# Kernel optimization log

Measured on AMD Instinct MI355X. Metric: run time of the kernel, lower is better.

The kernel has to match this reference:

```python
import jax, jax.numpy as jnp
import numpy as np
import math

DIM = 1024
N_HEADS = 16
HEAD_DIM = DIM // N_HEADS


def rope(x):
    # x: [B, H, S, D] with D == HEAD_DIM, interleaved even/odd rotation
    S = x.shape[-2]
    D = x.shape[-1]
    pos = jnp.arange(S, dtype=x.dtype)[:, None]              # [S, 1]
    dim = jnp.arange(D // 2, dtype=x.dtype)[None, :]         # [1, D/2]
    theta = pos / jnp.exp(2.0 * dim / D * math.log(10000.0))  # [S, D/2]
    sin = jnp.sin(theta)[None, None]                          # [1,1,S,D/2]
    cos = jnp.cos(theta)[None, None]
    x1 = x[..., ::2]
    x2 = x[..., 1::2]
    out1 = x1 * cos - x2 * sin
    out2 = x1 * sin + x2 * cos
    # interleave back: stack on last axis then flatten pairs
    return jnp.stack([out1, out2], axis=-1).reshape(x.shape)


def setup_inputs() -> dict:
    key = jax.random.key(0)
    ks = jax.random.split(key, 9)
    B, S = 2, 2048
    s = 1.0 / math.sqrt(DIM)
    inp = {
        "x": jax.random.normal(ks[0], (B, S, DIM), dtype=jnp.float32),
        "wq": jax.random.normal(ks[1], (DIM, DIM), dtype=jnp.float32) * s,
        "bq": jnp.zeros((DIM,), dtype=jnp.float32),
        "wk": jax.random.normal(ks[2], (DIM, DIM), dtype=jnp.float32) * s,
        "bk": jnp.zeros((DIM,), dtype=jnp.float32),
        "wv": jax.random.normal(ks[3], (DIM, DIM), dtype=jnp.float32) * s,
        "bv": jnp.zeros((DIM,), dtype=jnp.float32),
        "wo": jax.random.normal(ks[4], (DIM, DIM), dtype=jnp.float32) * s,
        "bo": jnp.zeros((DIM,), dtype=jnp.float32),
    }
    return inp


def reference(x, wq, bq, wk, bk, wv, bv, wo, bo):
    B, S, _ = x.shape
    # torch Linear: y = x @ W^T + b
    def proj(w, b):
        y = jnp.einsum('bsd,ed->bse', x, w) + b
        return y.reshape(B, S, N_HEADS, HEAD_DIM).transpose(0, 2, 1, 3)  # [B,H,S,Dh]
    q = rope(proj(wq, bq))
    k = rope(proj(wk, bk))
    v = proj(wv, bv)
    score = jnp.einsum('bhqd,bhkd->bhqk', q, k) / math.sqrt(HEAD_DIM)
    causal = jnp.tril(jnp.ones((S, S), dtype=bool))
    score = jnp.where(causal[None, None], score, -jnp.inf)
    attn = jax.nn.softmax(score, axis=-1)
    out = jnp.einsum('bhqk,bhkd->bhqd', attn, v)
    out = out.transpose(0, 2, 1, 3).reshape(B, S, DIM)
    return jnp.einsum('bsd,ed->bse', out, wo) + bo
```

## Files before the change

kernel.cpp:

```cpp
#include <hip/hip_runtime.h>
#include <cstdint>
#include <cstddef>


typedef __bf16 bf16_t;
typedef __bf16 bf16x8 __attribute__((ext_vector_type(8)));
typedef __bf16 bf16x4 __attribute__((ext_vector_type(4)));
typedef float  f32x4  __attribute__((ext_vector_type(4)));

#define DEVFN __device__ __forceinline__

static constexpr int Bn  = 2;
static constexpr int S   = 2048;
static constexpr int DIM = 1024;
static constexpr int NH  = 16;
static constexpr int HD  = 64;
static constexpr int Mrows = Bn * S;

DEVFN f32x4 mfma16(bf16x8 a, bf16x8 b, f32x4 c) {
  return __builtin_amdgcn_mfma_f32_16x16x32_bf16(a, b, c, 0, 0, 0);
}

DEVFN void gl_lds16(const bf16_t* g, bf16_t* l) {
  __builtin_amdgcn_global_load_lds(
      (const __attribute__((address_space(1))) unsigned*)g,
      (__attribute__((address_space(3))) unsigned*)l, 16, 0, 0);
}

__global__ __launch_bounds__(256) void k_prep(
    const float* __restrict__ x, const float* __restrict__ wq,
    const float* __restrict__ wk, const float* __restrict__ wv,
    const float* __restrict__ wo, bf16_t* __restrict__ xb,
    bf16_t* __restrict__ wqb, bf16_t* __restrict__ wkb,
    bf16_t* __restrict__ wvb, bf16_t* __restrict__ wob,
    float2* __restrict__ tab) {
  const int bid = blockIdx.x;
  if (bid < 8192) {
    const float* src;
    bf16_t* dst;
    size_t base;
    if (bid < 4096) {
      src = x; dst = xb; base = (size_t)bid << 10;
    } else {
      int wsel = (bid - 4096) >> 10;
      src = wsel == 0 ? wq : wsel == 1 ? wk : wsel == 2 ? wv : wo;
      dst = wsel == 0 ? wqb : wsel == 1 ? wkb : wsel == 2 ? wvb : wob;
      base = (size_t)((bid - 4096) & 1023) << 10;
    }
    size_t i = base + (size_t)threadIdx.x * 4;
    float4 v = *(const float4*)(src + i);
    bf16x4 o = { (bf16_t)v.x, (bf16_t)v.y, (bf16_t)v.z, (bf16_t)v.w };
    *(bf16x4*)(dst + i) = o;
  } else {
    int i = (bid - 8192) * 256 + threadIdx.x;
    int s = i >> 5, d = i & 31;
    float th = (float)s * expf((float)d * -0.2878231366f);
    tab[i] = make_float2(cosf(th), sinf(th));
  }
}

__global__ __launch_bounds__(256) void k_rope(bf16_t* __restrict__ X,
                                              const float2* __restrict__ tab,
                                              float scale) {
  int i = blockIdx.x * 256 + threadIdx.x;
  int row = i >> 7;
  int s = row & (S - 1);
  int dd = (i & 7) << 3;
  int p0 = dd >> 1;
  bf16x8 v = *(bf16x8*)(X + (size_t)i * 8);
  bf16x8 o;
#pragma unroll
  for (int j = 0; j < 4; ++j) {
    float x1 = (float)v[2 * j], x2 = (float)v[2 * j + 1];
    float2 cs = tab[s * 32 + p0 + j];
    o[2 * j]     = (bf16_t)((x1 * cs.x - x2 * cs.y) * scale);
    o[2 * j + 1] = (bf16_t)((x1 * cs.y + x2 * cs.x) * scale);
  }
  *(bf16x8*)(X + (size_t)i * 8) = o;
}

__global__ __launch_bounds__(256) void k_trans(const bf16_t* __restrict__ Vin,
                                               bf16_t* __restrict__ VT) {
  __shared__ __align__(16) bf16_t tile[64][72];
  int s0 = blockIdx.x * 64, bh = blockIdx.y;
  int b = bh >> 4, h = bh & 15;
  int t = threadIdx.x;
#pragma unroll
  for (int it = 0; it < 2; ++it) {
    int sl = (t >> 3) + it * 32, d0 = (t & 7) << 3;
    *(bf16x8*)&tile[sl][d0] =
        *(const bf16x8*)(Vin + (size_t)(b * S + s0 + sl) * DIM + h * HD + d0);
  }
  __syncthreads();
  int d = t >> 2, c0 = (t & 3) * 16;
  bf16_t buf[16];
#pragma unroll
  for (int j = 0; j < 16; ++j) buf[j] = tile[c0 + j][d];
  bf16_t* op = VT + ((size_t)bh * HD + d) * S + s0 + c0;
  *(bf16x8*)op = *(bf16x8*)&buf[0];
  *(bf16x8*)(op + 8) = *(bf16x8*)&buf[8];
}

DEVFN void stage64(const bf16_t* __restrict__ A, const bf16_t* __restrict__ Bw,
                   bf16_t* Al, bf16_t* Bl, int m0, int n0, int k0, int t,
                   int w) {
#pragma unroll
  for (int ld = 0; ld < 4; ++ld) {
    int c = t + ld * 256;
    int row = c >> 3;
    int j = ((c & 7) ^ (row & 7)) << 3;
    bf16_t* dstA = Al + (size_t)(w * 64 + ld * 256) * 8;
    bf16_t* dstB = Bl + (size_t)(w * 64 + ld * 256) * 8;
    gl_lds16(A + (size_t)(m0 + row) * DIM + k0 + j, dstA);
    gl_lds16(Bw + (size_t)(n0 + row) * DIM + k0 + j, dstB);
  }
}

__global__ __launch_bounds__(256) void k_gemm_qkv(
    const bf16_t* __restrict__ A, const bf16_t* __restrict__ Wall,
    const float* __restrict__ c0, const float* __restrict__ c1,
    const float* __restrict__ c2, bf16_t* __restrict__ Oq,
    bf16_t* __restrict__ Ok, bf16_t* __restrict__ Ov_) {
  __shared__ __align__(16) bf16_t Al[128 * 64];
  __shared__ __align__(16) bf16_t Bl[128 * 64];
  const int t = threadIdx.x, w = t >> 6, l = t & 63;
  const int lr = l & 15, lc = l >> 4;
  const int lid = blockIdx.x;
  const int xcd = lid & 7, s = lid >> 3;
  const int my = ((xcd >> 1) << 3) + (s & 7);
  const int nx = (xcd & 1) * 12 + (s >> 3);
  const int m0 = my * 128, n0g = nx * 128;
  const int z = n0g >> 10, n0l = n0g & 1023;
  const int wr = w >> 1, wc = w & 1;
  f32x4 acc[4][4] = {};

  for (int k0 = 0; k0 < DIM; k0 += 64) {
    __syncthreads();
    stage64(A, Wall, Al, Bl, m0, n0g, k0, t, w);
    asm volatile("s_waitcnt vmcnt(0)" ::: "memory");
    __syncthreads();
    bf16x8 af[2][4], bfr[2][4];
#pragma unroll
    for (int ks = 0; ks < 2; ++ks) {
#pragma unroll
      for (int mi = 0; mi < 4; ++mi) {
        int row = wr * 64 + mi * 16 + lr;
        int off = ((ks * 4 + lc) << 4) ^ ((row & 7) << 4);
        af[ks][mi] = *(const bf16x8*)((const char*)Al + row * 128 + off);
      }
#pragma unroll
      for (int ni = 0; ni < 4; ++ni) {
        int row = wc * 64 + ni * 16 + lr;
        int off = ((ks * 4 + lc) << 4) ^ ((row & 7) << 4);
        bfr[ks][ni] = *(const bf16x8*)((const char*)Bl + row * 128 + off);
      }
    }
    __builtin_amdgcn_s_setprio(1);
#pragma unroll
    for (int ks = 0; ks < 2; ++ks)
#pragma unroll
      for (int mi = 0; mi < 4; ++mi)
#pragma unroll
        for (int ni = 0; ni < 4; ++ni)
          acc[mi][ni] = mfma16(af[ks][mi], bfr[ks][ni], acc[mi][ni]);
    __builtin_amdgcn_s_setprio(0);
  }

  bf16_t* Ov = z == 0 ? Oq : (z == 1 ? Ok : Ov_);
  const float* bias = z == 0 ? c0 : (z == 1 ? c1 : c2);
#pragma unroll
  for (int ni = 0; ni < 4; ++ni) {
    const int col = n0l + wc * 64 + ni * 16 + lr;
    const float bv = bias[col];
#pragma unroll
    for (int mi = 0; mi < 4; ++mi)
#pragma unroll
      for (int r = 0; r < 4; ++r) {
        int row = m0 + wr * 64 + mi * 16 + lc * 4 + r;
        Ov[(size_t)row * DIM + col] = (bf16_t)(acc[mi][ni][r] + bv);
      }
  }
}

__global__ __launch_bounds__(256) void k_gemm_out(
    const bf16_t* __restrict__ A, const bf16_t* __restrict__ Bw,
    const float* __restrict__ bias, float* __restrict__ Ov) {
  __shared__ __align__(16) bf16_t Al[128 * 64];
  __shared__ __align__(16) bf16_t Bl[128 * 64];
  const int t = threadIdx.x, w = t >> 6, l = t & 63;
  const int lr = l & 15, lc = l >> 4;
  const int lid = blockIdx.x;
  const int xcd = lid & 7, s = lid >> 3;
  const int my = ((xcd >> 1) << 3) + (s & 7);
  const int nx = (xcd & 1) * 4 + (s >> 3);
  const int m0 = my * 128, n0 = nx * 128;
  const int wr = w >> 1, wc = w & 1;
  f32x4 acc[4][4] = {};

  for (int k0 = 0; k0 < DIM; k0 += 64) {
    __syncthreads();
    stage64(A, Bw, Al, Bl, m0, n0, k0, t, w);
    asm volatile("s_waitcnt vmcnt(0)" ::: "memory");
    __syncthreads();
    bf16x8 af[2][4], bfr[2][4];
#pragma unroll
    for (int ks = 0; ks < 2; ++ks) {
#pragma unroll
      for (int mi = 0; mi < 4; ++mi) {
        int row = wr * 64 + mi * 16 + lr;
        int off = ((ks * 4 + lc) << 4) ^ ((row & 7) << 4);
        af[ks][mi] = *(const bf16x8*)((const char*)Al + row * 128 + off);
      }
#pragma unroll
      for (int ni = 0; ni < 4; ++ni) {
        int row = wc * 64 + ni * 16 + lr;
        int off = ((ks * 4 + lc) << 4) ^ ((row & 7) << 4);
        bfr[ks][ni] = *(const bf16x8*)((const char*)Bl + row * 128 + off);
      }
    }
    __builtin_amdgcn_s_setprio(1);
#pragma unroll
    for (int ks = 0; ks < 2; ++ks)
#pragma unroll
      for (int mi = 0; mi < 4; ++mi)
#pragma unroll
        for (int ni = 0; ni < 4; ++ni)
          acc[mi][ni] = mfma16(af[ks][mi], bfr[ks][ni], acc[mi][ni]);
    __builtin_amdgcn_s_setprio(0);
  }

#pragma unroll
  for (int ni = 0; ni < 4; ++ni) {
    int col = n0 + wc * 64 + ni * 16 + lr;
    float bv = bias[col];
#pragma unroll
    for (int mi = 0; mi < 4; ++mi)
#pragma unroll
      for (int r = 0; r < 4; ++r) {
        int row = m0 + wr * 64 + mi * 16 + lc * 4 + r;
        Ov[(size_t)row * DIM + col] = acc[mi][ni][r] + bv;
      }
  }
}

DEVFN void stage_kv(const bf16_t* __restrict__ Kc,
                    const bf16_t* __restrict__ VT, bf16_t* Kb, bf16_t* Vb,
                    int b, int bh, int h, int k0, int tid, int w) {
#pragma unroll
  for (int ld = 0; ld < 2; ++ld) {
    int c = tid + ld * 256;
    int row = c >> 3;
    int j = ((c & 7) ^ (row & 7)) << 3;
    bf16_t* dstK = Kb + (size_t)(w * 64 + ld * 256) * 8;
    bf16_t* dstV = Vb + (size_t)(w * 64 + ld * 256) * 8;
    gl_lds16(Kc + (size_t)(b * S + k0 + row) * DIM + h * HD + j, dstK);
    gl_lds16(VT + ((size_t)bh * HD + row) * S + k0 + j, dstV);
  }
}

__global__ __launch_bounds__(256) void k_attn(const bf16_t* __restrict__ Q,
                                              const bf16_t* __restrict__ Kc,
                                              const bf16_t* __restrict__ VT,
                                              bf16_t* __restrict__ O) {
  __shared__ __align__(16) bf16_t Kl[2][64 * 64];
  __shared__ __align__(16) bf16_t Vl[3][64 * 64];
  __shared__ __align__(16) bf16_t Pl[4][16 * 64];
  const int tid = threadIdx.x, w = tid >> 6, l = tid & 63;
  const int lr = l & 15, lc = l >> 4;
  const int lid = blockIdx.x + (blockIdx.y << 4);
  const int xcd = lid & 7, slot = lid >> 3;
  const int bh = xcd * 4 + (slot >> 4);
  const int a = slot & 15;
  const int b = bh >> 4, h = bh & 15;
  char* Pw = (char*)&Pl[w][0];

#pragma unroll 1
  for (int pi = 0; pi < 2; ++pi) {
    const int tile = (pi == 0) ? a : 31 - a;
    const int q0 = tile * 64;
    const int nt = tile + 1;

    bf16x8 qf[2];
    {
      const bf16_t* qp =
          Q + (size_t)(b * S + q0 + w * 16 + lr) * DIM + h * HD + lc * 8;
      qf[0] = *(const bf16x8*)qp;
      qf[1] = *(const bf16x8*)(qp + 32);
    }
    f32x4 o[4] = {};
    f32x4 sA[4], sB[4];
    float m_run = -INFINITY;
    float rowsum = 0.f;

    auto qkt = [&](f32x4(&sd)[4], const bf16_t* Kb) {
#pragma unroll
      for (int ni = 0; ni < 4; ++ni) sd[ni] = f32x4{0.f, 0.f, 0.f, 0.f};
      __builtin_amdgcn_s_setprio(1);
#pragma unroll
      for (int ks = 0; ks < 2; ++ks)
#pragma unroll
        for (int ni = 0; ni < 4; ++ni) {
          int row = ni * 16 + lr;
          int off = (ks * 64 + lc * 16) ^ ((row & 7) << 4);
          bf16x8 kf = *(const bf16x8*)((const char*)Kb + row * 128 + off);
          sd[ni] = mfma16(kf, qf[ks], sd[ni]);
        }
      __builtin_amdgcn_s_setprio(0);
    };

    stage_kv(Kc, VT, &Kl[0][0], &Vl[0][0], b, bh, h, 0, tid, w);
    if (nt > 1) {
      stage_kv(Kc, VT, &Kl[1][0], &Vl[1][0], b, bh, h, 64, tid, w);
      asm volatile("s_waitcnt vmcnt(4)" ::: "memory");
    } else {
      asm volatile("s_waitcnt vmcnt(0)" ::: "memory");
    }
    __builtin_amdgcn_s_barrier();
    __builtin_amdgcn_sched_barrier(0);
    qkt(sA, &Kl[0][0]);
    __builtin_amdgcn_s_barrier();

    auto body = [&](f32x4(&scur)[4], f32x4(&snxt)[4], int t) {
      if (t + 2 < nt)
        stage_kv(Kc, VT, &Kl[(t + 2) & 1][0], &Vl[(t + 2) % 3][0], b, bh, h,
                 (t + 2) * 64, tid, w);
      if (t + 1 < nt) {
        if (t + 2 < nt)
          asm volatile("s_waitcnt vmcnt(4)" ::: "memory");
        else
          asm volatile("s_waitcnt vmcnt(0)" ::: "memory");
        __builtin_amdgcn_s_barrier();
        __builtin_amdgcn_sched_barrier(0);
        qkt(snxt, &Kl[(t + 1) & 1][0]);
      }

      if (t == nt - 1) {
        const int qloc = w * 16 + lr;
#pragma unroll
        for (int ni = 0; ni < 4; ++ni)
#pragma unroll
          for (int r = 0; r < 4; ++r)
            if (ni * 16 + lc * 4 + r > qloc) scur[ni][r] = -INFINITY;
      }

      float pm = scur[0][0];
#pragma unroll
      for (int ni = 0; ni < 4; ++ni)
#pragma unroll
        for (int r = 0; r < 4; ++r) pm = fmaxf(pm, scur[ni][r]);
      pm = fmaxf(pm, __shfl_xor(pm, 16));
      pm = fmaxf(pm, __shfl_xor(pm, 32));

      if (__ballot(pm > m_run + 8.f)) {
        float mn = fmaxf(m_run, pm);
        float alpha = __expf(m_run - mn);
        m_run = mn;
        rowsum *= alpha;
#pragma unroll
        for (int r = 0; r < 4; ++r) {
          float aq = __shfl(alpha, lc * 4 + r);
#pragma unroll
          for (int ni = 0; ni < 4; ++ni) o[ni][r] *= aq;
        }
      }

      float rs = 0.f;
#pragma unroll
      for (int ni = 0; ni < 4; ++ni) {
        float p0 = __expf(scur[ni][0] - m_run);
        float p1 = __expf(scur[ni][1] - m_run);
        float p2 = __expf(scur[ni][2] - m_run);
        float p3 = __expf(scur[ni][3] - m_run);
        rs += (p0 + p1) + (p2 + p3);
        bf16x4 pb = { (bf16_t)p0, (bf16_t)p1, (bf16_t)p2, (bf16_t)p3 };
        *(bf16x4*)(Pw + (lr * 128 + ((ni * 32 + lc * 8) ^ ((lr & 7) << 4)))) =
            pb;
      }
      rs += __shfl_xor(rs, 16);
      rs += __shfl_xor(rs, 32);
      rowsum += rs;

      const bf16_t* Vb = &Vl[t % 3][0];
      __builtin_amdgcn_s_setprio(1);
#pragma unroll
      for (int ks = 0; ks < 2; ++ks) {
        int off = ks * 64 + lc * 16;
        bf16x8 pa = *(const bf16x8*)(Pw + lr * 128 + (off ^ ((lr & 7) << 4)));
#pragma unroll
        for (int ni = 0; ni < 4; ++ni) {
          int vrow = ni * 16 + lr;
          bf16x8 vb = *(const bf16x8*)((const char*)Vb + vrow * 128 +
                                       (off ^ ((vrow & 7) << 4)));
          o[ni] = mfma16(pa, vb, o[ni]);
        }
      }
      __builtin_amdgcn_s_setprio(0);

      __builtin_amdgcn_s_barrier();
    };

#pragma unroll 1
    for (int t = 0; t < nt; ++t) {
      if (t & 1)
        body(sB, sA, t);
      else
        body(sA, sB, t);
    }

    float inv[4];
#pragma unroll
    for (int r = 0; r < 4; ++r) inv[r] = 1.0f / __shfl(rowsum, lc * 4 + r);
#pragma unroll
    for (int ni = 0; ni < 4; ++ni)
#pragma unroll
      for (int r = 0; r < 4; ++r) {
        int qr = q0 + w * 16 + lc * 4 + r;
        float v = o[ni][r] * inv[r];
        O[(size_t)(b * S + qr) * DIM + h * HD + ni * 16 + lr] = (bf16_t)v;
      }
  }
}

extern "C" void kernel_launch(void* const* d_in, const int* in_sizes, int n_in,
                              void* d_out, int out_size, void* d_ws,
                              size_t ws_size, hipStream_t stream) {
  const float* x  = (const float*)d_in[0];
  const float* wq = (const float*)d_in[1];
  const float* bq = (const float*)d_in[2];
  const float* wk = (const float*)d_in[3];
  const float* bk = (const float*)d_in[4];
  const float* wv = (const float*)d_in[5];
  const float* bv = (const float*)d_in[6];
  const float* wo = (const float*)d_in[7];
  const float* bo = (const float*)d_in[8];

  const size_t MD = (size_t)Mrows * DIM;
  const size_t WD = (size_t)DIM * DIM;
  bf16_t* W = (bf16_t*)d_ws;
  bf16_t* x_bf  = W;
  bf16_t* wq_bf = x_bf + MD;
  bf16_t* wk_bf = wq_bf + WD;
  bf16_t* wv_bf = wk_bf + WD;
  bf16_t* wo_bf = wv_bf + WD;
  bf16_t* q_lin = wo_bf + WD;
  bf16_t* k_lin = q_lin + MD;
  bf16_t* v_lin = k_lin + MD;
  bf16_t* vT    = v_lin + MD;
  float2* tab   = (float2*)(vT + MD);
  bf16_t* attn_out = x_bf;

  k_prep<<<8448, 256, 0, stream>>>(x, wq, wk, wv, wo, x_bf, wq_bf, wk_bf,
                                   wv_bf, wo_bf, tab);

  k_gemm_qkv<<<768, 256, 0, stream>>>(x_bf, wq_bf, bq, bk, bv, q_lin, k_lin,
                                      v_lin);

  k_rope<<<2048, 256, 0, stream>>>(q_lin, tab, 0.125f);
  k_rope<<<2048, 256, 0, stream>>>(k_lin, tab, 1.0f);
  k_trans<<<dim3(S / 64, Bn * NH), 256, 0, stream>>>(v_lin, vT);

  k_attn<<<dim3(16, Bn * NH), 256, 0, stream>>>(q_lin, k_lin, vT, attn_out);

  k_gemm_out<<<256, 256, 0, stream>>>(attn_out, wo_bf, bo, (float*)d_out);
}
```

Before: 132.9 us.

## Simplify attention pipeline to double buffering and use exp2 with log2e-folded scale

Replaces the attention loop's software pipeline, which staged K/V two tiles ahead with triple-buffered V and computed QK^T one tile ahead, with a plain double-buffered loop. Each iteration prefetches the next tile, waits, then does QK^T, softmax and PV. It also folds log2(e) into the Q scaling in the rope pass so the softmax can use exp2 instead of exp. This cuts shared memory use and register pressure, but QK^T no longer overlaps the previous tile's softmax and there is less prefetch distance.

```diff
diff --git a/kernel.cpp b/kernel.cpp
--- a/kernel.cpp
+++ b/kernel.cpp
@@ -1,6 +1,7 @@
 #include <hip/hip_runtime.h>
 #include <cstdint>
 #include <cstddef>
+#include <cmath>
 
 
 typedef __bf16 bf16_t;
@@ -26,6 +27,8 @@
       (const __attribute__((address_space(1))) unsigned*)g,
       (__attribute__((address_space(3))) unsigned*)l, 16, 0, 0);
 }
+
+DEVFN float fast_exp2(float x) { return exp2f(x); }
 
 __global__ __launch_bounds__(256) void k_prep(
     const float* __restrict__ x, const float* __restrict__ wq,
@@ -263,7 +266,7 @@
                                               const bf16_t* __restrict__ VT,
                                               bf16_t* __restrict__ O) {
   __shared__ __align__(16) bf16_t Kl[2][64 * 64];
-  __shared__ __align__(16) bf16_t Vl[3][64 * 64];
+  __shared__ __align__(16) bf16_t Vl[2][64 * 64];
   __shared__ __align__(16) bf16_t Pl[4][16 * 64];
   const int tid = threadIdx.x, w = tid >> 6, l = tid & 63;
   const int lr = l & 15, lc = l >> 4;
@@ -288,72 +291,60 @@
       qf[1] = *(const bf16x8*)(qp + 32);
     }
     f32x4 o[4] = {};
-    f32x4 sA[4], sB[4];
     float m_run = -INFINITY;
     float rowsum = 0.f;
 
-    auto qkt = [&](f32x4(&sd)[4], const bf16_t* Kb) {
-#pragma unroll
-      for (int ni = 0; ni < 4; ++ni) sd[ni] = f32x4{0.f, 0.f, 0.f, 0.f};
+    stage_kv(Kc, VT, &Kl[0][0], &Vl[0][0], b, bh, h, 0, tid, w);
+
+#pragma unroll 1
+    for (int it = 0; it < nt; ++it) {
+      const int cur = it & 1;
+      const bf16_t* Kb = &Kl[cur][0];
+      const bf16_t* Vb = &Vl[cur][0];
+      if (it + 1 < nt) {
+        stage_kv(Kc, VT, &Kl[cur ^ 1][0], &Vl[cur ^ 1][0], b, bh, h,
+                 (it + 1) * 64, tid, w);
+        asm volatile("s_waitcnt vmcnt(4)" ::: "memory");
+      } else {
+        asm volatile("s_waitcnt vmcnt(0)" ::: "memory");
+      }
+      __builtin_amdgcn_s_barrier();
+      __builtin_amdgcn_sched_barrier(0);
+
+      f32x4 s[4] = {};
       __builtin_amdgcn_s_setprio(1);
 #pragma unroll
-      for (int ks = 0; ks < 2; ++ks)
+      for (int ks = 0; ks < 2; ++ks) {
 #pragma unroll
         for (int ni = 0; ni < 4; ++ni) {
           int row = ni * 16 + lr;
           int off = (ks * 64 + lc * 16) ^ ((row & 7) << 4);
           bf16x8 kf = *(const bf16x8*)((const char*)Kb + row * 128 + off);
-          sd[ni] = mfma16(kf, qf[ks], sd[ni]);
+          s[ni] = mfma16(kf, qf[ks], s[ni]);
         }
+      }
       __builtin_amdgcn_s_setprio(0);
-    };
-
-    stage_kv(Kc, VT, &Kl[0][0], &Vl[0][0], b, bh, h, 0, tid, w);
-    if (nt > 1) {
-      stage_kv(Kc, VT, &Kl[1][0], &Vl[1][0], b, bh, h, 64, tid, w);
-      asm volatile("s_waitcnt vmcnt(4)" ::: "memory");
-    } else {
-      asm volatile("s_waitcnt vmcnt(0)" ::: "memory");
-    }
-    __builtin_amdgcn_s_barrier();
-    __builtin_amdgcn_sched_barrier(0);
-    qkt(sA, &Kl[0][0]);
-    __builtin_amdgcn_s_barrier();
-
-    auto body = [&](f32x4(&scur)[4], f32x4(&snxt)[4], int t) {
-      if (t + 2 < nt)
-        stage_kv(Kc, VT, &Kl[(t + 2) & 1][0], &Vl[(t + 2) % 3][0], b, bh, h,
-                 (t + 2) * 64, tid, w);
-      if (t + 1 < nt) {
-        if (t + 2 < nt)
-          asm volatile("s_waitcnt vmcnt(4)" ::: "memory");
-        else
-          asm volatile("s_waitcnt vmcnt(0)" ::: "memory");
-        __builtin_amdgcn_s_barrier();
-        __builtin_amdgcn_sched_barrier(0);
-        qkt(snxt, &Kl[(t + 1) & 1][0]);
-      }
-
-      if (t == nt - 1) {
+
+      if (it == tile) {
         const int qloc = w * 16 + lr;
 #pragma unroll
         for (int ni = 0; ni < 4; ++ni)
 #pragma unroll
           for (int r = 0; r < 4; ++r)
-            if (ni * 16 + lc * 4 + r > qloc) scur[ni][r] = -INFINITY;
-      }
-
-      float pm = scur[0][0];
-#pragma unroll
-      for (int ni = 0; ni < 4; ++ni)
-#pragma unroll
-        for (int r = 0; r < 4; ++r) pm = fmaxf(pm, scur[ni][r]);
+            if (ni * 16 + lc * 4 + r > qloc) s[ni][r] = -INFINITY;
+      }
+
+      float m01 = fmaxf(fmaxf(s[0][0], s[0][1]), fmaxf(s[0][2], s[0][3]));
+      float m23 = fmaxf(fmaxf(s[1][0], s[1][1]), fmaxf(s[1][2], s[1][3]));
+      float m45 = fmaxf(fmaxf(s[2][0], s[2][1]), fmaxf(s[2][2], s[2][3]));
+      float m67 = fmaxf(fmaxf(s[3][0], s[3][1]), fmaxf(s[3][2], s[3][3]));
+      float pm = fmaxf(fmaxf(m01, m23), fmaxf(m45, m67));
       pm = fmaxf(pm, __shfl_xor(pm, 16));
       pm = fmaxf(pm, __shfl_xor(pm, 32));
 
       if (__ballot(pm > m_run + 8.f)) {
         float mn = fmaxf(m_run, pm);
-        float alpha = __expf(m_run - mn);
+        float alpha = fast_exp2(m_run - mn);
         m_run = mn;
         rowsum *= alpha;
 #pragma unroll
@@ -367,10 +358,10 @@
       float rs = 0.f;
 #pragma unroll
       for (int ni = 0; ni < 4; ++ni) {
-        float p0 = __expf(scur[ni][0] - m_run);
-        float p1 = __expf(scur[ni][1] - m_run);
-        float p2 = __expf(scur[ni][2] - m_run);
-        float p3 = __expf(scur[ni][3] - m_run);
+        float p0 = fast_exp2(s[ni][0] - m_run);
+        float p1 = fast_exp2(s[ni][1] - m_run);
+        float p2 = fast_exp2(s[ni][2] - m_run);
+        float p3 = fast_exp2(s[ni][3] - m_run);
         rs += (p0 + p1) + (p2 + p3);
         bf16x4 pb = { (bf16_t)p0, (bf16_t)p1, (bf16_t)p2, (bf16_t)p3 };
         *(bf16x4*)(Pw + (lr * 128 + ((ni * 32 + lc * 8) ^ ((lr & 7) << 4)))) =
@@ -380,12 +371,12 @@
       rs += __shfl_xor(rs, 32);
       rowsum += rs;
 
-      const bf16_t* Vb = &Vl[t % 3][0];
       __builtin_amdgcn_s_setprio(1);
 #pragma unroll
       for (int ks = 0; ks < 2; ++ks) {
         int off = ks * 64 + lc * 16;
-        bf16x8 pa = *(const bf16x8*)(Pw + lr * 128 + (off ^ ((lr & 7) << 4)));
+        bf16x8 pa =
+            *(const bf16x8*)(Pw + lr * 128 + (off ^ ((lr & 7) << 4)));
 #pragma unroll
         for (int ni = 0; ni < 4; ++ni) {
           int vrow = ni * 16 + lr;
@@ -397,14 +388,6 @@
       __builtin_amdgcn_s_setprio(0);
 
       __builtin_amdgcn_s_barrier();
-    };
-
-#pragma unroll 1
-    for (int t = 0; t < nt; ++t) {
-      if (t & 1)
-        body(sB, sA, t);
-      else
-        body(sA, sB, t);
     }
 
     float inv[4];
@@ -455,7 +438,7 @@
   k_gemm_qkv<<<768, 256, 0, stream>>>(x_bf, wq_bf, bq, bk, bv, q_lin, k_lin,
                                       v_lin);
 
-  k_rope<<<2048, 256, 0, stream>>>(q_lin, tab, 0.125f);
+  k_rope<<<2048, 256, 0, stream>>>(q_lin, tab, 0.125f * 1.4426950408889634f);
   k_rope<<<2048, 256, 0, stream>>>(k_lin, tab, 1.0f);
   k_trans<<<dim3(S / 64, Bn * NH), 256, 0, stream>>>(v_lin, vT);
 
```

Result: no change. 134.3 us (+1.1%).
